# Kernel optimization log

Measured on AMD Instinct MI355X. Metric: run time of the kernel, lower is better.

Reference implementation:

```python
import jax, jax.numpy as jnp
import numpy as np

N, E, IN_DIM, OUT_DIM, T = 100000, 1600000, 128, 64, 8
V_THRESHOLD = 1.0
EPS = 1e-7

# ---- Lorentz manifold (curvature -1), time coordinate first ----

def _linner(a, b):
    # Lorentzian inner product <a,b>_L = -a0*b0 + sum_i ai*bi
    return -a[..., 0] * b[..., 0] + jnp.sum(a[..., 1:] * b[..., 1:], axis=-1)

def _proju(z, u):
    # project ambient vector u to tangent space at z (<z,z>_L = -1)
    return u + _linner(z, u)[..., None] * z

def _expmap(z, u):
    un = jnp.sqrt(jnp.maximum(_linner(u, u), EPS))[..., None]
    return jnp.cosh(un) * z + jnp.sinh(un) * u / un

def _dist0(z):
    # geodesic distance to origin o=(1,0,...,0): arccosh(-<o,z>_L) = arccosh(z0)
    return jnp.arccosh(jnp.maximum(z[..., 0], 1.0 + EPS))

# ---- GCNConv (torch_geometric semantics: self-loops + symmetric norm) ----

def _gcn(x, edge_index, W, b):
    src, dst = edge_index[0], edge_index[1]
    loops = jnp.arange(N, dtype=src.dtype)
    src = jnp.concatenate([src, loops])
    dst = jnp.concatenate([dst, loops])
    deg = jax.ops.segment_sum(jnp.ones_like(dst, dtype=x.dtype), dst, num_segments=N)
    dinv = jax.lax.rsqrt(jnp.maximum(deg, 1.0))  # deg >= 1 due to self-loops
    norm = dinv[src] * dinv[dst]                 # [E+N]
    h = x @ W                                    # [N, OUT_DIM]
    out = jax.ops.segment_sum(norm[:, None] * h[src], dst, num_segments=N)
    return out + b


def setup_inputs() -> dict:
    key = jax.random.key(0)
    k1, k2, k3 = jax.random.split(key, 3)
    x = jax.random.normal(k1, (N, IN_DIM), dtype=jnp.float32)
    edge_index = jax.random.randint(k2, (2, E), 0, N, dtype=jnp.int32)
    W = jax.random.normal(k3, (IN_DIM, OUT_DIM), dtype=jnp.float32) / np.sqrt(IN_DIM)
    b = jnp.zeros((OUT_DIM,), dtype=jnp.float32)
    return {"x": x, "edge_index": edge_index, "W": W, "b": b}


def reference(x, edge_index, W, b):
    h = _gcn(x, edge_index, W, b)                       # [N, D]
    origin = jnp.zeros_like(h).at[..., 0].set(1.0)      # manifold origin
    x_seq = jnp.broadcast_to(h, (T,) + h.shape)         # [T, N, D]

    def step(z, x_t):
        u = _proju(z, x_t)                              # input current in T_z M
        z_new = _expmap(z, u)                           # charge along geodesic
        v = _dist0(z_new)                               # membrane potential [N]
        spike = v >= V_THRESHOLD
        z_out = jnp.where(spike[..., None], origin, z_new)  # hard reset
        return z_out, (spike.astype(h.dtype), z_out)

    _, (o_seq, z_seq) = jax.lax.scan(step, origin, x_seq)
    return o_seq, z_seq  # [T, N], [T, N, D]
```

## Files before the change

### kernel.cpp

```cpp
#include <hip/hip_runtime.h>
#include <math.h>

#define IN_DIM_C 128
#define OUT_DIM_C 64
#define T_STEPS 8
#define KC_MAX 512
#define PTILE 2048

__device__ __forceinline__ float4 f4zero() { return make_float4(0.f, 0.f, 0.f, 0.f); }

__global__ __launch_bounds__(256) void k_hist(const int* __restrict__ dst,
                                              int* __restrict__ chist, int E) {
    __shared__ int hh[KC_MAX];
    const int tid = threadIdx.x;
    for (int i = tid; i < KC_MAX; i += 256) hh[i] = 0;
    __syncthreads();
    long base = (long)blockIdx.x * 4096;
    #pragma unroll
    for (int j = 0; j < 16; ++j) {
        long e = base + j * 256 + tid;
        if (e < E) atomicAdd(&hh[dst[e] >> 8], 1);
    }
    __syncthreads();
    for (int i = tid; i < KC_MAX; i += 256)
        if (hh[i]) atomicAdd(&chist[i], hh[i]);
}

__global__ __launch_bounds__(64) void k_scanK(const int* __restrict__ chist,
                                              int* __restrict__ gcursor,
                                              int* __restrict__ offsets,
                                              int kc, int n, int E) {
    int lane = threadIdx.x;
    int carry = 0;
    for (int c = 0; c * 64 < kc; ++c) {
        int idx = c * 64 + lane;
        int v = (idx < kc) ? chist[idx] : 0;
        int x = v;
        #pragma unroll
        for (int off = 1; off < 64; off <<= 1) {
            int t = __shfl_up(x, off, 64);
            if (lane >= off) x += t;
        }
        if (idx < kc) gcursor[idx] = carry + x - v;
        carry += __shfl(x, 63, 64);
    }
    if (lane == 0) offsets[n] = E;
}

__global__ __launch_bounds__(256) void k_gemm(const float* __restrict__ x,
                                              const float* __restrict__ W,
                                              float* __restrict__ h,
                                              int n, int n_groups) {
    __shared__ __align__(16) float Ws[IN_DIM_C * OUT_DIM_C];
    __shared__ __align__(16) float xs[16 * 136];

    for (int i = threadIdx.x; i < IN_DIM_C * OUT_DIM_C / 4; i += 256)
        ((float4*)Ws)[i] = ((const float4*)W)[i];

    const int ln = threadIdx.x >> 4;
    const int dg = threadIdx.x & 15;
    const float4* Ws4 = (const float4*)Ws;

    for (int g = blockIdx.x; g < n_groups; g += gridDim.x) {
        int node_base = g * 16;
        __syncthreads();
        for (int f = threadIdx.x; f < 512; f += 256) {
            int row = f >> 5, c4 = f & 31;
            int node = node_base + row;
            float4 v = f4zero();
            if (node < n) v = *(const float4*)&x[(long)node * IN_DIM_C + c4 * 4];
            *(float4*)&xs[row * 136 + c4 * 4] = v;
        }
        __syncthreads();

        int node = node_base + ln;
        float4 acc = f4zero();
        #pragma unroll
        for (int k = 0; k < IN_DIM_C; k += 4) {
            float4 xv = *(const float4*)&xs[ln * 136 + k];
            float4 w0 = Ws4[(k + 0) * 16 + dg];
            float4 w1 = Ws4[(k + 1) * 16 + dg];
            float4 w2 = Ws4[(k + 2) * 16 + dg];
            float4 w3 = Ws4[(k + 3) * 16 + dg];
            acc.x = fmaf(xv.x, w0.x, acc.x); acc.y = fmaf(xv.x, w0.y, acc.y);
            acc.z = fmaf(xv.x, w0.z, acc.z); acc.w = fmaf(xv.x, w0.w, acc.w);
            acc.x = fmaf(xv.y, w1.x, acc.x); acc.y = fmaf(xv.y, w1.y, acc.y);
            acc.z = fmaf(xv.y, w1.z, acc.z); acc.w = fmaf(xv.y, w1.w, acc.w);
            acc.x = fmaf(xv.z, w2.x, acc.x); acc.y = fmaf(xv.z, w2.y, acc.y);
            acc.z = fmaf(xv.z, w2.z, acc.z); acc.w = fmaf(xv.z, w2.w, acc.w);
            acc.x = fmaf(xv.w, w3.x, acc.x); acc.y = fmaf(xv.w, w3.y, acc.y);
            acc.z = fmaf(xv.w, w3.z, acc.z); acc.w = fmaf(xv.w, w3.w, acc.w);
        }
        if (node < n)
            *(float4*)&h[(long)node * OUT_DIM_C + dg * 4] = acc;
    }
}

__global__ __launch_bounds__(256) void k_part(const int* __restrict__ src,
                                              const int* __restrict__ dst,
                                              int* __restrict__ gcursor,
                                              int* __restrict__ part, int E, int kc) {
    __shared__ int hist[KC_MAX];
    __shared__ int offs[KC_MAX];
    __shared__ int cur[KC_MAX];
    __shared__ int gbase[KC_MAX];
    const int tid = threadIdx.x;
    long base = (long)blockIdx.x * PTILE;

    for (int i = tid; i < KC_MAX; i += 256) hist[i] = 0;
    __syncthreads();
    #pragma unroll
    for (int j = 0; j < PTILE / 256; ++j) {
        long e = base + j * 256 + tid;
        if (e < E) atomicAdd(&hist[dst[e] >> 8], 1);
    }
    __syncthreads();
    if (tid < 64) {
        int carry = 0;
        for (int c = 0; c * 64 < kc; ++c) {
            int idx = c * 64 + tid;
            int v = (idx < kc) ? hist[idx] : 0;
            int x = v;
            #pragma unroll
            for (int off = 1; off < 64; off <<= 1) {
                int t = __shfl_up(x, off, 64);
                if (tid >= off) x += t;
            }
            if (idx < kc) { offs[idx] = carry + x - v; cur[idx] = carry + x - v; }
            carry += __shfl(x, 63, 64);
        }
    }
    __syncthreads();
    for (int b = tid; b < kc; b += 256)
        gbase[b] = hist[b] ? atomicAdd(&gcursor[b], hist[b]) : 0;
    __syncthreads();
    #pragma unroll
    for (int j = 0; j < PTILE / 256; ++j) {
        long e = base + j * 256 + tid;
        if (e < E) {
            int d = dst[e];
            int b = d >> 8;
            int r = atomicAdd(&cur[b], 1);
            part[gbase[b] + r - offs[b]] = (src[e] << 8) | (d & 255);
        }
    }
}

__global__ __launch_bounds__(256) void k_sort(const int* __restrict__ part,
                                              const int* __restrict__ gcursor,
                                              int* __restrict__ part2,
                                              int* __restrict__ offsets,
                                              float* __restrict__ dinv, int n) {
    __shared__ int cnt[256];
    __shared__ int cur[256];
    __shared__ int wsum[4], woff[4];
    const int tid = threadIdx.x;
    const int bkt = blockIdx.x;
    int start = bkt ? gcursor[bkt - 1] : 0;
    int end = gcursor[bkt];

    cnt[tid] = 0;
    __syncthreads();
    for (int i = start + tid; i < end; i += 256)
        atomicAdd(&cnt[part[i] & 255], 1);
    __syncthreads();

    int v = cnt[tid];
    int lane = tid & 63, wv = tid >> 6;
    int x = v;
    #pragma unroll
    for (int off = 1; off < 64; off <<= 1) {
        int t = __shfl_up(x, off, 64);
        if (lane >= off) x += t;
    }
    if (lane == 63) wsum[wv] = x;
    __syncthreads();
    if (tid == 0) { int c = 0; for (int w = 0; w < 4; ++w) { woff[w] = c; c += wsum[w]; } }
    __syncthreads();
    int myloc = woff[wv] + x - v;
    cur[tid] = myloc;
    int node = (bkt << 8) + tid;
    if (node < n) {
        offsets[node] = start + myloc;
        dinv[node] = rsqrtf((float)(v + 1));
    }
    __syncthreads();

    for (int i = start + tid; i < end; i += 256) {
        int p = part[i];
        int r = atomicAdd(&cur[p & 255], 1);
        part2[start + r] = ((unsigned)p) >> 8;
    }
}

__global__ __launch_bounds__(256) void k_pull(const int* __restrict__ offsets,
                                              const int* __restrict__ part2,
                                              const float* __restrict__ dinv,
                                              const float* __restrict__ h,
                                              const float* __restrict__ b,
                                              float* __restrict__ agg, int n) {
    int node = (blockIdx.x * 256 + threadIdx.x) >> 6;
    int lane = threadIdx.x & 63;
    if (node >= n) return;
    int o0 = offsets[node], o1 = offsets[node + 1];
    float dd = dinv[node];
    float acc = fmaf(dd * dd, h[(long)node * OUT_DIM_C + lane], b[lane]);
    int i = o0;
    for (; i + 4 <= o1; i += 4) {
        int s0 = part2[i], s1 = part2[i + 1], s2 = part2[i + 2], s3 = part2[i + 3];
        float n0 = dinv[s0] * dd, n1 = dinv[s1] * dd, n2 = dinv[s2] * dd, n3 = dinv[s3] * dd;
        acc = fmaf(n0, h[(long)s0 * OUT_DIM_C + lane], acc);
        acc = fmaf(n1, h[(long)s1 * OUT_DIM_C + lane], acc);
        acc = fmaf(n2, h[(long)s2 * OUT_DIM_C + lane], acc);
        acc = fmaf(n3, h[(long)s3 * OUT_DIM_C + lane], acc);
    }
    for (; i < o1; ++i) {
        int s = part2[i];
        acc = fmaf(dinv[s] * dd, h[(long)s * OUT_DIM_C + lane], acc);
    }
    agg[(long)node * OUT_DIM_C + lane] = acc;
}

__global__ __launch_bounds__(256) void k_spike(const float* agg,
                                               float* o_seq, float* z_seq, int n) {
    int gid = blockIdx.x * 256 + threadIdx.x;
    int node = gid >> 4;
    int sub = threadIdx.x & 15;
    if (node >= n) return;
    const float s0 = (sub == 0) ? -1.0f : 1.0f;
    int lane0 = (threadIdx.x & 63) & ~15;

    float4 g = *(const float4*)&agg[(long)node * OUT_DIM_C + sub * 4];
    float4 origin = f4zero();
    if (sub == 0) origin.x = 1.0f;

    auto step = [&](float4 z, float4& zn, bool& sp) {
        float p = s0 * z.x * g.x + z.y * g.y + z.z * g.z + z.w * g.w;
        p += __shfl_xor(p, 1, 64);
        p += __shfl_xor(p, 2, 64);
        p += __shfl_xor(p, 4, 64);
        p += __shfl_xor(p, 8, 64);
        float4 u = make_float4(fmaf(p, z.x, g.x), fmaf(p, z.y, g.y),
                               fmaf(p, z.z, g.z), fmaf(p, z.w, g.w));
        float q = s0 * u.x * u.x + u.y * u.y + u.z * u.z + u.w * u.w;
        q += __shfl_xor(q, 1, 64);
        q += __shfl_xor(q, 2, 64);
        q += __shfl_xor(q, 4, 64);
        q += __shfl_xor(q, 8, 64);
        float un = sqrtf(fmaxf(q, 1e-7f));
        float c = coshf(un);
        float sh = sinhf(un) / un;
        zn = make_float4(fmaf(c, z.x, sh * u.x), fmaf(c, z.y, sh * u.y),
                         fmaf(c, z.z, sh * u.z), fmaf(c, z.w, sh * u.w));
        float z0 = __shfl(zn.x, lane0, 64);
        float v = acoshf(fmaxf(z0, 1.0f + 1e-7f));
        sp = (v >= 1.0f);
    };

    float4 z1; bool sp0;
    step(origin, z1, sp0);
    float4 r0 = sp0 ? origin : z1;

    float4 z = origin;
    bool at0 = true;
    for (int t = 0; t < T_STEPS; ++t) {
        float4 zn; bool sp;
        if (at0) { sp = sp0; zn = r0; }
        else {
            step(z, zn, sp);
            if (sp) zn = origin;
        }
        *(float4*)&z_seq[(long)t * n * OUT_DIM_C + (long)node * OUT_DIM_C + sub * 4] = zn;
        if (sub == 0) o_seq[(long)t * n + node] = sp ? 1.0f : 0.0f;
        z = zn;
        at0 = sp;
    }
}

extern "C" void kernel_launch(void* const* d_in, const int* in_sizes, int n_in,
                              void* d_out, int out_size, void* d_ws, size_t ws_size,
                              hipStream_t stream) {
    const float* x  = (const float*)d_in[0];
    const int*   ei = (const int*)d_in[1];
    const float* W  = (const float*)d_in[2];
    const float* b  = (const float*)d_in[3];
    const int N = in_sizes[0] / IN_DIM_C;
    const int E = in_sizes[1] / 2;
    const int KC = (N + 255) >> 8;

    float* out   = (float*)d_out;
    float* o_seq = out;
    float* z_seq = out + (long)T_STEPS * N;

    float* agg     = z_seq;
    float* h       = z_seq + 1L * N * OUT_DIM_C;
    int*   part    = (int*)(z_seq + 2L * N * OUT_DIM_C);
    int*   part2   = (int*)(z_seq + 3L * N * OUT_DIM_C);
    int*   chist   = (int*)(z_seq + 4L * N * OUT_DIM_C);
    int*   gcursor = chist + KC_MAX;
    int*   offsets = gcursor + KC_MAX;
    float* dinv    = (float*)(offsets + N + 1);

    const int* srcp = ei;
    const int* dstp = ei + E;

    hipMemsetAsync(chist, 0, (size_t)KC_MAX * sizeof(int), stream);
    k_hist<<<(E + 4095) / 4096, 256, 0, stream>>>(dstp, chist, E);
    k_scanK<<<1, 64, 0, stream>>>(chist, gcursor, offsets, KC, N, E);

    int n_groups = (N + 15) / 16;
    k_gemm<<<1024, 256, 0, stream>>>(x, W, h, N, n_groups);

    k_part<<<(E + PTILE - 1) / PTILE, 256, 0, stream>>>(srcp, dstp, gcursor, part, E, KC);
    k_sort<<<KC, 256, 0, stream>>>(part, gcursor, part2, offsets, dinv, N);
    k_pull<<<(N * 64 + 255) / 256, 256, 0, stream>>>(offsets, part2, dinv, h, b, agg, N);

    k_spike<<<(N + 15) / 16, 256, 0, stream>>>(agg, o_seq, z_seq, N);
}
```

Measured before the change: 433.4 us.

## Fuse GCN pull aggregation with Lorentz spiking dynamics using workspace buffers

Adds a kernel that performs the neighbor aggregation and the spiking time loop in one pass, with one wavefront per node, so the aggregated features never round-trip through global memory. To make this possible without overwriting scratch data stored in the output, intermediates move into the workspace when it is large enough, with the old two-kernel path kept as a fallback. The gather loop is also unrolled to 8 edges with loads batched ahead of the FMAs for more memory-level parallelism. The spike step now uses full 64-lane shuffle reductions instead of 16-lane float4 groups, which adds shuffle work per time step.

```diff
diff --git a/kernel.cpp b/kernel.cpp
--- a/kernel.cpp
+++ b/kernel.cpp
@@ -193,6 +193,79 @@
     }
 }
 
+__global__ __launch_bounds__(256) void k_pullspike(const int* __restrict__ offsets,
+                                                   const int* __restrict__ part2,
+                                                   const float* __restrict__ dinv,
+                                                   const float* __restrict__ h,
+                                                   const float* __restrict__ b,
+                                                   float* __restrict__ o_seq,
+                                                   float* __restrict__ z_seq, int n) {
+    int node = (blockIdx.x * 256 + threadIdx.x) >> 6;
+    int lane = threadIdx.x & 63;
+    if (node >= n) return;
+
+    int o0 = offsets[node], o1 = offsets[node + 1];
+    float dd = dinv[node];
+    float g = fmaf(dd * dd, h[(long)node * OUT_DIM_C + lane], b[lane]);
+    int i = o0;
+    for (; i + 8 <= o1; i += 8) {
+        int s[8]; float nr[8], hv[8];
+        #pragma unroll
+        for (int k = 0; k < 8; ++k) s[k] = part2[i + k];
+        #pragma unroll
+        for (int k = 0; k < 8; ++k) hv[k] = h[(long)s[k] * OUT_DIM_C + lane];
+        #pragma unroll
+        for (int k = 0; k < 8; ++k) nr[k] = dinv[s[k]] * dd;
+        #pragma unroll
+        for (int k = 0; k < 8; ++k) g = fmaf(nr[k], hv[k], g);
+    }
+    for (; i < o1; ++i) {
+        int s = part2[i];
+        g = fmaf(dinv[s] * dd, h[(long)s * OUT_DIM_C + lane], g);
+    }
+
+    const float s0 = (lane == 0) ? -1.0f : 1.0f;
+    const float zo = (lane == 0) ? 1.0f : 0.0f;
+
+    auto step = [&](float z, float& zn, bool& sp) {
+        float p = s0 * z * g;
+        p += __shfl_xor(p, 1, 64);  p += __shfl_xor(p, 2, 64);
+        p += __shfl_xor(p, 4, 64);  p += __shfl_xor(p, 8, 64);
+        p += __shfl_xor(p, 16, 64); p += __shfl_xor(p, 32, 64);
+        float u = fmaf(p, z, g);
+        float q = s0 * u * u;
+        q += __shfl_xor(q, 1, 64);  q += __shfl_xor(q, 2, 64);
+        q += __shfl_xor(q, 4, 64);  q += __shfl_xor(q, 8, 64);
+        q += __shfl_xor(q, 16, 64); q += __shfl_xor(q, 32, 64);
+        float un = sqrtf(fmaxf(q, 1e-7f));
+        float c = coshf(un);
+        float sh = sinhf(un) / un;
+        zn = fmaf(c, z, sh * u);
+        float z0 = __shfl(zn, 0, 64);
+        float v = acoshf(fmaxf(z0, 1.0f + 1e-7f));
+        sp = (v >= 1.0f);
+    };
+
+    float z1; bool sp0;
+    step(zo, z1, sp0);
+    float r0 = sp0 ? zo : z1;
+
+    float z = zo;
+    bool at0 = true;
+    for (int t = 0; t < T_STEPS; ++t) {
+        float zn; bool sp;
+        if (at0) { sp = sp0; zn = r0; }
+        else {
+            step(z, zn, sp);
+            if (sp) zn = zo;
+        }
+        z_seq[(long)t * n * OUT_DIM_C + (long)node * OUT_DIM_C + lane] = zn;
+        if (lane == 0) o_seq[(long)t * n + node] = sp ? 1.0f : 0.0f;
+        z = zn;
+        at0 = sp;
+    }
+}
+
 __global__ __launch_bounds__(256) void k_pull(const int* __restrict__ offsets,
                                               const int* __restrict__ part2,
                                               const float* __restrict__ dinv,
@@ -206,13 +279,14 @@
     float dd = dinv[node];
     float acc = fmaf(dd * dd, h[(long)node * OUT_DIM_C + lane], b[lane]);
     int i = o0;
-    for (; i + 4 <= o1; i += 4) {
-        int s0 = part2[i], s1 = part2[i + 1], s2 = part2[i + 2], s3 = part2[i + 3];
-        float n0 = dinv[s0] * dd, n1 = dinv[s1] * dd, n2 = dinv[s2] * dd, n3 = dinv[s3] * dd;
-        acc = fmaf(n0, h[(long)s0 * OUT_DIM_C + lane], acc);
-        acc = fmaf(n1, h[(long)s1 * OUT_DIM_C + lane], acc);
-        acc = fmaf(n2, h[(long)s2 * OUT_DIM_C + lane], acc);
-        acc = fmaf(n3, h[(long)s3 * OUT_DIM_C + lane], acc);
+    for (; i + 8 <= o1; i += 8) {
+        int s[8]; float hv[8];
+        #pragma unroll
+        for (int k = 0; k < 8; ++k) s[k] = part2[i + k];
+        #pragma unroll
+        for (int k = 0; k < 8; ++k) hv[k] = h[(long)s[k] * OUT_DIM_C + lane];
+        #pragma unroll
+        for (int k = 0; k < 8; ++k) acc = fmaf(dinv[s[k]] * dd, hv[k], acc);
     }
     for (; i < o1; ++i) {
         int s = part2[i];
@@ -223,55 +297,47 @@
 
 __global__ __launch_bounds__(256) void k_spike(const float* agg,
                                                float* o_seq, float* z_seq, int n) {
-    int gid = blockIdx.x * 256 + threadIdx.x;
-    int node = gid >> 4;
-    int sub = threadIdx.x & 15;
+    int node = (blockIdx.x * 256 + threadIdx.x) >> 6;
+    int lane = threadIdx.x & 63;
     if (node >= n) return;
-    const float s0 = (sub == 0) ? -1.0f : 1.0f;
-    int lane0 = (threadIdx.x & 63) & ~15;
-
-    float4 g = *(const float4*)&agg[(long)node * OUT_DIM_C + sub * 4];
-    float4 origin = f4zero();
-    if (sub == 0) origin.x = 1.0f;
-
-    auto step = [&](float4 z, float4& zn, bool& sp) {
-        float p = s0 * z.x * g.x + z.y * g.y + z.z * g.z + z.w * g.w;
-        p += __shfl_xor(p, 1, 64);
-        p += __shfl_xor(p, 2, 64);
-        p += __shfl_xor(p, 4, 64);
-        p += __shfl_xor(p, 8, 64);
-        float4 u = make_float4(fmaf(p, z.x, g.x), fmaf(p, z.y, g.y),
-                               fmaf(p, z.z, g.z), fmaf(p, z.w, g.w));
-        float q = s0 * u.x * u.x + u.y * u.y + u.z * u.z + u.w * u.w;
-        q += __shfl_xor(q, 1, 64);
-        q += __shfl_xor(q, 2, 64);
-        q += __shfl_xor(q, 4, 64);
-        q += __shfl_xor(q, 8, 64);
+    float g = agg[(long)node * OUT_DIM_C + lane];
+    const float s0 = (lane == 0) ? -1.0f : 1.0f;
+    const float zo = (lane == 0) ? 1.0f : 0.0f;
+
+    auto step = [&](float z, float& zn, bool& sp) {
+        float p = s0 * z * g;
+        p += __shfl_xor(p, 1, 64);  p += __shfl_xor(p, 2, 64);
+        p += __shfl_xor(p, 4, 64);  p += __shfl_xor(p, 8, 64);
+        p += __shfl_xor(p, 16, 64); p += __shfl_xor(p, 32, 64);
+        float u = fmaf(p, z, g);
+        float q = s0 * u * u;
+        q += __shfl_xor(q, 1, 64);  q += __shfl_xor(q, 2, 64);
+        q += __shfl_xor(q, 4, 64);  q += __shfl_xor(q, 8, 64);
+        q += __shfl_xor(q, 16, 64); q += __shfl_xor(q, 32, 64);
         float un = sqrtf(fmaxf(q, 1e-7f));
         float c = coshf(un);
         float sh = sinhf(un) / un;
-        zn = make_float4(fmaf(c, z.x, sh * u.x), fmaf(c, z.y, sh * u.y),
-                         fmaf(c, z.z, sh * u.z), fmaf(c, z.w, sh * u.w));
-        float z0 = __shfl(zn.x, lane0, 64);
+        zn = fmaf(c, z, sh * u);
+        float z0 = __shfl(zn, 0, 64);
         float v = acoshf(fmaxf(z0, 1.0f + 1e-7f));
         sp = (v >= 1.0f);
     };
 
-    float4 z1; bool sp0;
-    step(origin, z1, sp0);
-    float4 r0 = sp0 ? origin : z1;
-
-    float4 z = origin;
+    float z1; bool sp0;
+    step(zo, z1, sp0);
+    float r0 = sp0 ? zo : z1;
+
+    float z = zo;
     bool at0 = true;
     for (int t = 0; t < T_STEPS; ++t) {
-        float4 zn; bool sp;
+        float zn; bool sp;
         if (at0) { sp = sp0; zn = r0; }
         else {
             step(z, zn, sp);
-            if (sp) zn = origin;
-        }
-        *(float4*)&z_seq[(long)t * n * OUT_DIM_C + (long)node * OUT_DIM_C + sub * 4] = zn;
-        if (sub == 0) o_seq[(long)t * n + node] = sp ? 1.0f : 0.0f;
+            if (sp) zn = zo;
+        }
+        z_seq[(long)t * n * OUT_DIM_C + (long)node * OUT_DIM_C + lane] = zn;
+        if (lane == 0) o_seq[(long)t * n + node] = sp ? 1.0f : 0.0f;
         z = zn;
         at0 = sp;
     }
@@ -292,17 +358,29 @@
     float* o_seq = out;
     float* z_seq = out + (long)T_STEPS * N;
 
-    float* agg     = z_seq;
-    float* h       = z_seq + 1L * N * OUT_DIM_C;
-    int*   part    = (int*)(z_seq + 2L * N * OUT_DIM_C);
-    int*   part2   = (int*)(z_seq + 3L * N * OUT_DIM_C);
-    int*   chist   = (int*)(z_seq + 4L * N * OUT_DIM_C);
-    int*   gcursor = chist + KC_MAX;
-    int*   offsets = gcursor + KC_MAX;
-    float* dinv    = (float*)(offsets + N + 1);
-
     const int* srcp = ei;
     const int* dstp = ei + E;
+
+    const long n_h = (long)N * OUT_DIM_C;
+    const long n_meta = 2L * KC_MAX + (N + 1) + N;
+    const size_t need = (size_t)(n_h + 2L * E + n_meta) * 4;
+
+    float *h; int *part, *part2, *chist, *gcursor, *offsets; float *dinv;
+    bool fused = (ws_size >= need);
+    if (fused) {
+        h       = (float*)d_ws;
+        part    = (int*)(h + n_h);
+        part2   = part + E;
+        chist   = part2 + E;
+    } else {
+        h       = z_seq + 1L * n_h;
+        part    = (int*)(z_seq + 2L * n_h);
+        part2   = (int*)(z_seq + 3L * n_h);
+        chist   = (int*)(z_seq + 4L * n_h);
+    }
+    gcursor = chist + KC_MAX;
+    offsets = gcursor + KC_MAX;
+    dinv    = (float*)(offsets + N + 1);
 
     hipMemsetAsync(chist, 0, (size_t)KC_MAX * sizeof(int), stream);
     k_hist<<<(E + 4095) / 4096, 256, 0, stream>>>(dstp, chist, E);
@@ -313,7 +391,13 @@
 
     k_part<<<(E + PTILE - 1) / PTILE, 256, 0, stream>>>(srcp, dstp, gcursor, part, E, KC);
     k_sort<<<KC, 256, 0, stream>>>(part, gcursor, part2, offsets, dinv, N);
-    k_pull<<<(N * 64 + 255) / 256, 256, 0, stream>>>(offsets, part2, dinv, h, b, agg, N);
-
-    k_spike<<<(N + 15) / 16, 256, 0, stream>>>(agg, o_seq, z_seq, N);
-}
+
+    if (fused) {
+        k_pullspike<<<(N * 64 + 255) / 256, 256, 0, stream>>>(offsets, part2, dinv, h, b,
+                                                              o_seq, z_seq, N);
+    } else {
+        float* agg = z_seq;
+        k_pull<<<(N * 64 + 255) / 256, 256, 0, stream>>>(offsets, part2, dinv, h, b, agg, N);
+        k_spike<<<(N * 64 + 255) / 256, 256, 0, stream>>>(agg, o_seq, z_seq, N);
+    }
+}
```

Measured after the change: 444.6 us. 2.6% more time.
